# Optimization experiments

Hardware: AMD Instinct MI355X
Metric: run time of the kernel (lower is better)

Reference implementation:

```python
import jax, jax.numpy as jnp
from jax import lax
import numpy as np

BOHR = 0.52917721067  # Angstrom per Bohr (au.BOHR)
DAMP_MUTUAL = 0.39
DAMP_FIELD = 0.7
N_ITER = 7  # fixed-point iterations for induced dipoles


def setup_inputs() -> dict:
    key = jax.random.key(0)
    N = 100000
    deg = 32
    E = N * deg
    k1, k2, k3, k4, k5, k6, k7 = jax.random.split(key, 7)
    edge_src = jax.random.randint(k1, (E,), 0, N)
    edge_dst = jax.random.randint(k2, (E,), 0, N)
    # realistic interatomic distances in [1, 6] Angstrom (avoid r ~ 0)
    distances = 1.0 + 5.0 * jax.random.uniform(k3, (E,), dtype=jnp.float32)
    u = jax.random.normal(k4, (E, 3), dtype=jnp.float32)
    u = u / jnp.linalg.norm(u, axis=-1, keepdims=True)
    vec = u * distances[:, None]  # consistent |vec| == distances
    polarisability = 0.5 + 1.5 * jax.random.uniform(k5, (N,), dtype=jnp.float32)
    charges = 0.3 * jax.random.normal(k6, (N,), dtype=jnp.float32)
    species = jax.random.randint(k7, (N,), 1, 10)
    return {
        "species": species,
        "edge_src": edge_src,
        "edge_dst": edge_dst,
        "distances": distances,
        "vec": vec,
        "polarisability": polarisability,
        "charges": charges,
    }


def reference(species, edge_src, edge_dst, distances, vec, polarisability, charges):
    N = polarisability.shape[0]
    # convert to atomic units
    rij = distances / BOHR                      # [E]
    vec_ij = vec / BOHR                         # [E,3]
    pol = polarisability.reshape(-1) / BOHR**3  # [N]

    # Thole damping: u_ij^3 = r^3 / sqrt(alpha_i * alpha_j)
    alpha_ij = pol[edge_src] * pol[edge_dst]
    uij3 = rij**3 / jnp.sqrt(alpha_ij)
    exp_m = jnp.exp(-DAMP_MUTUAL * uij3)
    l3_m = 1.0 - exp_m
    l5_m = 1.0 - (1.0 + DAMP_MUTUAL * uij3) * exp_m
    l3_f = 1.0 - jnp.exp(-DAMP_FIELD * uij3)

    inv_r3 = 1.0 / rij**3
    inv_r5 = inv_r3 / rij**2

    # permanent (charge) electric field at src atoms, Thole-damped
    e_edges = (l3_f * charges[edge_dst] * inv_r3)[:, None] * vec_ij  # [E,3]
    E0 = jax.ops.segment_sum(e_edges, edge_src, num_segments=N)      # [N,3]

    alpha = pol[:, None]  # isotropic polarisability [N,1]

    def matvec(mu):
        # Thole-damped dipole-dipole interaction tensor applied to mu: (T mu)_i
        mu_d = mu[edge_dst]                                   # [E,3]
        dot = jnp.sum(vec_ij * mu_d, axis=-1)                 # [E]
        t = (l3_m * inv_r3)[:, None] * mu_d \
            - (3.0 * l5_m * inv_r5 * dot)[:, None] * vec_ij   # [E,3]
        return jax.ops.segment_sum(t, edge_src, num_segments=N)

    # iterative induced dipoles: mu = alpha * (E0 - T mu)
    mu0 = alpha * E0

    def step(mu, _):
        return alpha * (E0 - matvec(mu)), None

    mu, _ = lax.scan(step, mu0, None, length=N_ITER)

    # per-atom polarisation energy: -1/2 mu . E0
    energy = -0.5 * jnp.sum(mu * E0, axis=-1)  # [N]
    return energy
```

## Files before the change

### kernel.cpp

```cpp
#include <hip/hip_runtime.h>
#include <hip/hip_fp16.h>


static constexpr float INV_B  = 1.0f / 0.52917721067f;
static constexpr float INV_B3 = INV_B * INV_B * INV_B;
static constexpr float DM = 0.39f;
static constexpr float DF = 0.7f;
static constexpr int   NITER = 7;
#define SCAN_B 512
#define CHUNK 16384
#define BUILD_T 1024
#define MAXBUCK 512

__device__ inline unsigned packh2(float a, float b) {
    return (unsigned)__half_as_ushort(__float2half_rn(a)) |
           ((unsigned)__half_as_ushort(__float2half_rn(b)) << 16);
}
__device__ inline float unph_lo(unsigned u) {
    return __half2float(__ushort_as_half((unsigned short)(u & 0xFFFFu)));
}
__device__ inline float unph_hi(unsigned u) {
    return __half2float(__ushort_as_half((unsigned short)(u >> 16)));
}


__global__ void bhist_kernel(const int* __restrict__ esrc, int* __restrict__ hraw,
                             int* __restrict__ hpad, int E, int nbuck, int nblk)
{
    __shared__ int cnt[MAXBUCK];
    int tid = threadIdx.x, blk = blockIdx.x;
    for (int b = tid; b < nbuck; b += blockDim.x) cnt[b] = 0;
    __syncthreads();
    int lo = blk * CHUNK, hi = min(E, lo + CHUNK);
    for (int i = lo + tid; i < hi; i += blockDim.x)
        atomicAdd(&cnt[esrc[i] >> 8], 1);
    __syncthreads();
    for (int b = tid; b < nbuck; b += blockDim.x) {
        int c = cnt[b];
        hraw[b * nblk + blk] = c;
        hpad[b * nblk + blk] = (c + 7) & ~7;
    }
}


__global__ void scan1_kernel(const int* __restrict__ in, int* __restrict__ excl,
                             int* __restrict__ blocksum, int n)
{
    __shared__ int sh[SCAN_B];
    int tid = threadIdx.x;
    int i = blockIdx.x * SCAN_B + tid;
    int v = (i < n) ? in[i] : 0;
    sh[tid] = v;
    __syncthreads();
    for (int off = 1; off < SCAN_B; off <<= 1) {
        int t = (tid >= off) ? sh[tid - off] : 0;
        __syncthreads();
        sh[tid] += t;
        __syncthreads();
    }
    if (i < n) excl[i] = sh[tid] - v;
    if (tid == SCAN_B - 1) blocksum[blockIdx.x] = sh[tid];
}

__global__ void scan2_kernel(int* __restrict__ blocksum, int nb)
{
    __shared__ int sh[512];
    int tid = threadIdx.x;
    int v = (tid < nb) ? blocksum[tid] : 0;
    sh[tid] = v;
    __syncthreads();
    for (int off = 1; off < 512; off <<= 1) {
        int t = (tid >= off) ? sh[tid - off] : 0;
        __syncthreads();
        sh[tid] += t;
        __syncthreads();
    }
    if (tid < nb) blocksum[tid] = sh[tid] - v;
}

__global__ void scan3_kernel(int* __restrict__ excl, const int* __restrict__ blocksum, int n)
{
    int i = blockIdx.x * SCAN_B + threadIdx.x;
    if (i < n) excl[i] += blocksum[blockIdx.x];
}

__global__ void bktptr_kernel(const int* __restrict__ hoffpad, const int* __restrict__ hpad,
                              int* __restrict__ bktptr, int nbuck, int nblk, int nScan)
{
    int b = blockIdx.x * blockDim.x + threadIdx.x;
    if (b < nbuck) bktptr[b] = hoffpad[b * nblk];
    if (b == nbuck) bktptr[b] = hoffpad[nScan - 1] + hpad[nScan - 1];
}


__global__ void build_kernel(const int* __restrict__ esrc, const int* __restrict__ edst,
                             const float* __restrict__ dist, const float* __restrict__ vec,
                             const float* __restrict__ pol, const float* __restrict__ chg,
                             const int* __restrict__ hoffpad, const int* __restrict__ hpad,
                             uint4* __restrict__ recs, int E, int nbuck, int nblk)
{
    __shared__ int cur[MAXBUCK];
    int tid = threadIdx.x, blk = blockIdx.x;
    for (int b = tid; b < nbuck; b += blockDim.x) cur[b] = hoffpad[b * nblk + blk];
    __syncthreads();
    int lo = blk * CHUNK, hi = min(E, lo + CHUNK);
    for (int i = lo + tid; i < hi; i += blockDim.x) {
        int s = esrc[i], d = edst[i];
        float r  = dist[i] * INV_B;
        float vx = vec[3*i+0] * INV_B;
        float vy = vec[3*i+1] * INV_B;
        float vz = vec[3*i+2] * INV_B;
        float ps = pol[s] * INV_B3;
        float pd = pol[d] * INV_B3;
        float r2 = r * r;
        float r3 = r2 * r;
        float u  = r3 * rsqrtf(ps * pd);
        float em = __expf(-DM * u);
        float l3m = 1.0f - em;
        float l5m = 1.0f - (1.0f + DM * u) * em;
        float inv_r3 = 1.0f / r3;
        float inv_r5 = inv_r3 / r2;
        float c1 = l3m * inv_r3;
        float sw = sqrtf(3.0f * l5m * inv_r5);
        float ec = (1.0f - __expf(-DF * u)) * chg[d] * inv_r3;
        float g  = ec / sw;
        int slot = atomicAdd(&cur[s >> 8], 1);
        uint4 rc;
        rc.x = (unsigned)(d | ((s & 255) << 20));
        rc.y = __float_as_uint(c1);
        rc.z = packh2(sw * vx, sw * vy);
        rc.w = packh2(sw * vz, g);
        recs[slot] = rc;
    }
    __syncthreads();
    for (int b = tid; b < nbuck; b += blockDim.x) {
        int base = hoffpad[b * nblk + blk];
        int end  = base + hpad[b * nblk + blk];
        for (int s = cur[b]; s < end; ++s) recs[s] = make_uint4(0, 0, 0, 0);
    }
}


__global__ void sort_kernel(const int* __restrict__ bktptr, const int* __restrict__ hoffraw,
                            int nblk, const uint4* __restrict__ recs_raw,
                            unsigned* __restrict__ srt, float* __restrict__ gsrt,
                            int* __restrict__ rowbeg, int* __restrict__ rowend, int N)
{
    __shared__ int hist[256];
    __shared__ int scn[256];
    __shared__ int cur[256];
    int tid = threadIdx.x, b = blockIdx.x;
    int j0 = bktptr[b], j1 = bktptr[b + 1];
    int tight0 = hoffraw[b * nblk];
    if (tid < 256) hist[tid] = 0;
    __syncthreads();
    for (int j = j0 + tid; j < j1; j += blockDim.x) {
        uint4 rc = recs_raw[j];
        if (rc.y) atomicAdd(&hist[rc.x >> 20], 1);
    }
    __syncthreads();
    if (tid < 256) scn[tid] = hist[tid];
    __syncthreads();
    for (int off = 1; off < 256; off <<= 1) {
        int t = 0;
        if (tid < 256 && tid >= off) t = scn[tid - off];
        __syncthreads();
        if (tid < 256) scn[tid] += t;
        __syncthreads();
    }
    if (tid < 256) {
        int cnt = hist[tid];
        int beg = tight0 + scn[tid] - cnt;
        cur[tid] = beg;
        int row = b * 256 + tid;
        if (row < N) { rowbeg[row] = beg; rowend[row] = beg + cnt; }
    }
    __syncthreads();
    for (int j = j0 + tid; j < j1; j += blockDim.x) {
        uint4 rc = recs_raw[j];
        if (rc.y) {
            int slot = atomicAdd(&cur[rc.x >> 20], 1);
            float c1 = __uint_as_float(rc.y);
            float wx = unph_lo(rc.z);
            srt[3*slot+0] = rc.x;
            srt[3*slot+1] = packh2(c1, wx);
            srt[3*slot+2] = rc.w;
            srt[3*slot+2] = packh2(unph_hi(rc.z), unph_lo(rc.w));
            gsrt[slot] = unph_hi(rc.w);
        }
    }
}


__global__ void e0g_kernel(const int* __restrict__ rowbeg, const int* __restrict__ rowend,
                           const unsigned* __restrict__ srt, const float* __restrict__ gsrt,
                           const float* __restrict__ pol,
                           float4* __restrict__ E0, float4* __restrict__ mu, int N)
{
    int tid  = threadIdx.x;
    int lane = tid & 15;
    int row  = (blockIdx.x * blockDim.x + tid) >> 4;
    if (row >= N) return;
    int r0 = rowbeg[row], r1 = rowend[row];
    float sx = 0.f, sy = 0.f, sz = 0.f;
    for (int j = r0 + lane; j < r1; j += 16) {
        unsigned w0 = srt[3*j+1];
        unsigned w1 = srt[3*j+2];
        float g = gsrt[j];
        sx += g * unph_hi(w0);
        sy += g * unph_lo(w1);
        sz += g * unph_hi(w1);
    }
    for (int m = 8; m >= 1; m >>= 1) {
        sx += __shfl_xor(sx, m);
        sy += __shfl_xor(sy, m);
        sz += __shfl_xor(sz, m);
    }
    if (lane == 0) {
        E0[row] = make_float4(sx, sy, sz, 0.f);
        float a = pol[row] * INV_B3;
        mu[row] = make_float4(a * sx, a * sy, a * sz, 0.f);
    }
}

__global__ void mvg_kernel(const int* __restrict__ rowbeg, const int* __restrict__ rowend,
                           const unsigned* __restrict__ srt, const float4* __restrict__ E0,
                           const float* __restrict__ pol,
                           const float4* __restrict__ mu_in, float4* __restrict__ mu_out,
                           float* __restrict__ energy, int N, int final_iter)
{
    int tid  = threadIdx.x;
    int lane = tid & 15;
    int row  = (blockIdx.x * blockDim.x + tid) >> 4;
    if (row >= N) return;
    int r0 = rowbeg[row], r1 = rowend[row];
    float ax = 0.f, ay = 0.f, az = 0.f;
    for (int j = r0 + lane; j < r1; j += 16) {
        unsigned pk = srt[3*j+0];
        unsigned w0 = srt[3*j+1];
        unsigned w1 = srt[3*j+2];
        float4 m = mu_in[pk & 0xFFFFF];
        float c1 = unph_lo(w0);
        float wx = unph_hi(w0), wy = unph_lo(w1), wz = unph_hi(w1);
        float dot = wx * m.x + wy * m.y + wz * m.z;
        ax += c1 * m.x - dot * wx;
        ay += c1 * m.y - dot * wy;
        az += c1 * m.z - dot * wz;
    }
    for (int msk = 8; msk >= 1; msk >>= 1) {
        ax += __shfl_xor(ax, msk);
        ay += __shfl_xor(ay, msk);
        az += __shfl_xor(az, msk);
    }
    if (lane == 0) {
        float4 e0 = E0[row];
        float a = pol[row] * INV_B3;
        float mx = a * (e0.x - ax);
        float my = a * (e0.y - ay);
        float mz = a * (e0.z - az);
        mu_out[row] = make_float4(mx, my, mz, 0.f);
        if (final_iter)
            energy[row] = -0.5f * (mx * e0.x + my * e0.y + mz * e0.z);
    }
}


__global__ void e0b_kernel(const int* __restrict__ bktptr, const uint4* __restrict__ recs,
                           const float* __restrict__ pol,
                           float4* __restrict__ E0, float4* __restrict__ mu, int N)
{
    __shared__ float acc[256 * 3];
    int tid = threadIdx.x, b = blockIdx.x;
    for (int k = tid; k < 768; k += 256) acc[k] = 0.f;
    __syncthreads();
    int j0 = bktptr[b], j1 = bktptr[b + 1];
    for (int j = j0 + tid; j < j1; j += 256) {
        uint4 rc = recs[j];
        int lr = (int)(rc.x >> 20) & 255;
        float g = unph_hi(rc.w);
        atomicAdd(&acc[lr*3+0], g * unph_lo(rc.z));
        atomicAdd(&acc[lr*3+1], g * unph_hi(rc.z));
        atomicAdd(&acc[lr*3+2], g * unph_lo(rc.w));
    }
    __syncthreads();
    int r = b * 256 + tid;
    if (r < N) {
        float ax = acc[tid*3], ay = acc[tid*3+1], az = acc[tid*3+2];
        E0[r] = make_float4(ax, ay, az, 0.f);
        float a = pol[r] * INV_B3;
        mu[r] = make_float4(a * ax, a * ay, a * az, 0.f);
    }
}

__global__ void mvb_kernel(const int* __restrict__ bktptr, const uint4* __restrict__ recs,
                           const float4* __restrict__ E0, const float* __restrict__ pol,
                           const float4* __restrict__ mu_in, float4* __restrict__ mu_out,
                           float* __restrict__ energy, int N, int final_iter)
{
    __shared__ float acc[256 * 3];
    int tid = threadIdx.x, b = blockIdx.x;
    for (int k = tid; k < 768; k += 256) acc[k] = 0.f;
    __syncthreads();
    int j0 = bktptr[b], j1 = bktptr[b + 1];
    for (int j = j0 + tid; j < j1; j += 256) {
        uint4 rc = recs[j];
        float4 m = mu_in[rc.x & 0xFFFFF];
        float c1 = __uint_as_float(rc.y);
        float wx = unph_lo(rc.z), wy = unph_hi(rc.z), wz = unph_lo(rc.w);
        float dot = wx * m.x + wy * m.y + wz * m.z;
        int lr = (int)(rc.x >> 20) & 255;
        atomicAdd(&acc[lr*3+0], c1 * m.x - dot * wx);
        atomicAdd(&acc[lr*3+1], c1 * m.y - dot * wy);
        atomicAdd(&acc[lr*3+2], c1 * m.z - dot * wz);
    }
    __syncthreads();
    int r = b * 256 + tid;
    if (r < N) {
        float4 e0 = E0[r];
        float a = pol[r] * INV_B3;
        float mx = a * (e0.x - acc[tid*3+0]);
        float my = a * (e0.y - acc[tid*3+1]);
        float mz = a * (e0.z - acc[tid*3+2]);
        mu_out[r] = make_float4(mx, my, mz, 0.f);
        if (final_iter)
            energy[r] = -0.5f * (mx * e0.x + my * e0.y + mz * e0.z);
    }
}


__global__ void fb_e0_kernel(const int* esrc, const int* edst, const float* dist,
                             const float* vec, const float* pol, const float* chg,
                             float4* E0, int E)
{
    int e = blockIdx.x * blockDim.x + threadIdx.x;
    if (e >= E) return;
    int s = esrc[e], d = edst[e];
    float r  = dist[e] * INV_B;
    float vx = vec[3*e+0]*INV_B, vy = vec[3*e+1]*INV_B, vz = vec[3*e+2]*INV_B;
    float r3 = r*r*r;
    float u  = r3 * rsqrtf(pol[s]*INV_B3 * pol[d]*INV_B3);
    float ec = (1.0f - __expf(-DF*u)) * chg[d] / r3;
    atomicAdd(&E0[s].x, ec*vx); atomicAdd(&E0[s].y, ec*vy); atomicAdd(&E0[s].z, ec*vz);
}

__global__ void fb_init_kernel(const float* pol, const float4* E0, float4* mu, float4* acc, int N)
{
    int i = blockIdx.x * blockDim.x + threadIdx.x;
    if (i >= N) return;
    float a = pol[i]*INV_B3; float4 e0 = E0[i];
    mu[i]  = make_float4(a*e0.x, a*e0.y, a*e0.z, 0.f);
    acc[i] = make_float4(0.f,0.f,0.f,0.f);
}

__global__ void fb_matvec_kernel(const int* esrc, const int* edst, const float* dist,
                                 const float* vec, const float* pol,
                                 const float4* mu, float4* acc, int E)
{
    int e = blockIdx.x * blockDim.x + threadIdx.x;
    if (e >= E) return;
    int s = esrc[e], d = edst[e];
    float r  = dist[e]*INV_B;
    float vx = vec[3*e+0]*INV_B, vy = vec[3*e+1]*INV_B, vz = vec[3*e+2]*INV_B;
    float r2 = r*r, r3 = r2*r;
    float u  = r3 * rsqrtf(pol[s]*INV_B3 * pol[d]*INV_B3);
    float em = __expf(-DM*u);
    float c1 = (1.0f - em) / r3;
    float c2 = 3.0f * (1.0f - (1.0f + DM*u)*em) / (r3*r2);
    float4 m = mu[d];
    float k = c2 * (vx*m.x + vy*m.y + vz*m.z);
    atomicAdd(&acc[s].x, c1*m.x - k*vx);
    atomicAdd(&acc[s].y, c1*m.y - k*vy);
    atomicAdd(&acc[s].z, c1*m.z - k*vz);
}

__global__ void fb_update_kernel(const float* pol, const float4* E0, float4* acc,
                                 float4* mu, float* energy, int N, int final_iter)
{
    int i = blockIdx.x * blockDim.x + threadIdx.x;
    if (i >= N) return;
    float a = pol[i]*INV_B3; float4 e0 = E0[i]; float4 ac = acc[i];
    float mx = a*(e0.x-ac.x), my = a*(e0.y-ac.y), mz = a*(e0.z-ac.z);
    mu[i]  = make_float4(mx,my,mz,0.f);
    acc[i] = make_float4(0.f,0.f,0.f,0.f);
    if (final_iter) energy[i] = -0.5f*(mx*e0.x + my*e0.y + mz*e0.z);
}


static inline size_t align_up(size_t x, size_t a) { return (x + a - 1) & ~(a - 1); }

extern "C" void kernel_launch(void* const* d_in, const int* in_sizes, int n_in,
                              void* d_out, int out_size, void* d_ws, size_t ws_size,
                              hipStream_t stream)
{
    const int*   esrc = (const int*)  d_in[1];
    const int*   edst = (const int*)  d_in[2];
    const float* dist = (const float*)d_in[3];
    const float* vec  = (const float*)d_in[4];
    const float* pol  = (const float*)d_in[5];
    const float* chg  = (const float*)d_in[6];
    const int E = in_sizes[1];
    const int N = in_sizes[5];
    float* out = (float*)d_out;

    const int nbuck = (N + 255) >> 8;
    const int nblk  = (E + CHUNK - 1) / CHUNK;
    const int nScan = nbuck * nblk;
    const int g1    = (nScan + SCAN_B - 1) / SCAN_B;
    const size_t Epad = (size_t)E + 7u * (size_t)nScan;

    char* ws = (char*)d_ws;
    size_t off = 0;
    auto carve = [&](size_t bytes) { size_t o = off; off = align_up(off + bytes, 256); return o; };
    size_t o_hpad    = carve((size_t)nScan * 4);
    size_t o_hoffpad = carve((size_t)nScan * 4);
    size_t o_bsum1   = carve(512 * 4);
    size_t o_bkt     = carve((size_t)(nbuck + 1) * 4);
    size_t o_E0      = carve((size_t)N * 16);
    size_t o_mua     = carve((size_t)N * 16);
    size_t o_mub     = carve((size_t)N * 16);
    size_t o_hraw    = carve((size_t)nScan * 4);
    size_t o_recsraw = carve(Epad * 16);
    size_t need_mid  = off;
    size_t o_hoffraw = carve((size_t)nScan * 4);
    size_t o_bsum2   = carve(512 * 4);
    size_t o_rowbeg  = carve((size_t)N * 4);
    size_t o_rowend  = carve((size_t)N * 4);
    size_t o_srt     = carve((size_t)E * 12);
    size_t o_gsrt    = carve((size_t)E * 4);
    size_t need_sort = off;

    bool shape_ok = (nbuck <= MAXBUCK) && (g1 <= 512) && (nbuck >= 1) && (N < (1 << 20));
    bool ok_sort = shape_ok && (ws_size >= need_sort);
    bool ok_mid  = shape_ok && (ws_size >= need_mid);

    if (ok_sort || ok_mid) {
        int*    hpad    = (int*)   (ws + o_hpad);
        int*    hoffpad = (int*)   (ws + o_hoffpad);
        int*    bsum1   = (int*)   (ws + o_bsum1);
        int*    bktptr  = (int*)   (ws + o_bkt);
        float4* E0      = (float4*)(ws + o_E0);
        float4* mu_a    = (float4*)(ws + o_mua);
        float4* mu_b    = (float4*)(ws + o_mub);
        int*    hraw    = (int*)   (ws + o_hraw);
        uint4*  recsraw = (uint4*) (ws + o_recsraw);

        bhist_kernel<<<nblk, BUILD_T, 0, stream>>>(esrc, hraw, hpad, E, nbuck, nblk);
        scan1_kernel<<<g1, SCAN_B, 0, stream>>>(hpad, hoffpad, bsum1, nScan);
        scan2_kernel<<<1, 512, 0, stream>>>(bsum1, g1);
        scan3_kernel<<<g1, SCAN_B, 0, stream>>>(hoffpad, bsum1, nScan);
        bktptr_kernel<<<(nbuck + 256) / 256, 256, 0, stream>>>(hoffpad, hpad, bktptr,
                                                               nbuck, nblk, nScan);
        build_kernel<<<nblk, BUILD_T, 0, stream>>>(esrc, edst, dist, vec, pol, chg,
                                                   hoffpad, hpad, recsraw, E, nbuck, nblk);

        if (ok_sort) {
            int*      hoffraw = (int*)     (ws + o_hoffraw);
            int*      bsum2   = (int*)     (ws + o_bsum2);
            int*      rowbeg  = (int*)     (ws + o_rowbeg);
            int*      rowend  = (int*)     (ws + o_rowend);
            unsigned* srt     = (unsigned*)(ws + o_srt);
            float*    gsrt    = (float*)   (ws + o_gsrt);

            scan1_kernel<<<g1, SCAN_B, 0, stream>>>(hraw, hoffraw, bsum2, nScan);
            scan2_kernel<<<1, 512, 0, stream>>>(bsum2, g1);
            scan3_kernel<<<g1, SCAN_B, 0, stream>>>(hoffraw, bsum2, nScan);
            sort_kernel<<<nbuck, 512, 0, stream>>>(bktptr, hoffraw, nblk, recsraw,
                                                   srt, gsrt, rowbeg, rowend, N);

            const int NG16 = (N + 15) / 16;
            e0g_kernel<<<NG16, 256, 0, stream>>>(rowbeg, rowend, srt, gsrt, pol, E0, mu_a, N);
            float4* min_ = mu_a; float4* mout_ = mu_b;
            for (int it = 0; it < NITER; ++it) {
                mvg_kernel<<<NG16, 256, 0, stream>>>(rowbeg, rowend, srt, E0, pol,
                                                     min_, mout_, out, N, it == NITER - 1);
                float4* t = min_; min_ = mout_; mout_ = t;
            }
        } else {
            e0b_kernel<<<nbuck, 256, 0, stream>>>(bktptr, recsraw, pol, E0, mu_a, N);
            float4* min_ = mu_a; float4* mout_ = mu_b;
            for (int it = 0; it < NITER; ++it) {
                mvb_kernel<<<nbuck, 256, 0, stream>>>(bktptr, recsraw, E0, pol,
                                                      min_, mout_, out, N, it == NITER - 1);
                float4* t = min_; min_ = mout_; mout_ = t;
            }
        }
    } else {
        float4* E0  = (float4*)(ws);
        float4* mu  = (float4*)(ws + (size_t)N * 16);
        float4* acc = (float4*)(ws + (size_t)N * 32);
        const int EB = 256, NB = 256;
        const int EG = (E + EB - 1) / EB;
        const int NG = (N + NB - 1) / NB;
        hipMemsetAsync(E0, 0, (size_t)N * 16, stream);
        fb_e0_kernel<<<EG, EB, 0, stream>>>(esrc, edst, dist, vec, pol, chg, E0, E);
        fb_init_kernel<<<NG, NB, 0, stream>>>(pol, E0, mu, acc, N);
        for (int it = 0; it < NITER; ++it) {
            fb_matvec_kernel<<<EG, EB, 0, stream>>>(esrc, edst, dist, vec, pol, mu, acc, E);
            fb_update_kernel<<<NG, NB, 0, stream>>>(pol, E0, acc, mu, out, N, it == NITER - 1);
        }
    }
}
```

Measured before the change: 336.6 us.

## Locally sort edges by bucket in shared memory before building records

The build kernel now builds a per-block histogram and prefix scan of source buckets, creates a shared-memory permutation, and processes edges in bucket order so each thread writes its record to a deterministic, contiguous slot. This replaces the scattered global stores ordered by atomics with mostly coalesced writes into each bucket's region, and the padding fill now uses a rounded-up count instead of the hpad array. The cost is an extra pass over esrc, roughly 40KB of shared memory per block that limits occupancy, and permuted (less coalesced) input reads. A redundant store in the sort kernel is also removed.

```diff
diff --git a/kernel.cpp b/kernel.cpp
--- a/kernel.cpp
+++ b/kernel.cpp
@@ -93,23 +93,58 @@
 }
 
 
-__global__ void build_kernel(const int* __restrict__ esrc, const int* __restrict__ edst,
-                             const float* __restrict__ dist, const float* __restrict__ vec,
-                             const float* __restrict__ pol, const float* __restrict__ chg,
-                             const int* __restrict__ hoffpad, const int* __restrict__ hpad,
-                             uint4* __restrict__ recs, int E, int nbuck, int nblk)
-{
-    __shared__ int cur[MAXBUCK];
+__global__ __launch_bounds__(BUILD_T)
+void build_kernel(const int* __restrict__ esrc, const int* __restrict__ edst,
+                  const float* __restrict__ dist, const float* __restrict__ vec,
+                  const float* __restrict__ pol, const float* __restrict__ chg,
+                  const int* __restrict__ hoffpad,
+                  uint4* __restrict__ recs, int E, int nbuck, int nblk)
+{
+    __shared__ unsigned short perm[CHUNK];
+    __shared__ int hist[MAXBUCK];
+    __shared__ int scn[MAXBUCK];
+    __shared__ int lscan[MAXBUCK];
+    __shared__ int lcur[MAXBUCK];
+    __shared__ int rbase[MAXBUCK];
     int tid = threadIdx.x, blk = blockIdx.x;
-    for (int b = tid; b < nbuck; b += blockDim.x) cur[b] = hoffpad[b * nblk + blk];
-    __syncthreads();
-    int lo = blk * CHUNK, hi = min(E, lo + CHUNK);
-    for (int i = lo + tid; i < hi; i += blockDim.x) {
-        int s = esrc[i], d = edst[i];
-        float r  = dist[i] * INV_B;
-        float vx = vec[3*i+0] * INV_B;
-        float vy = vec[3*i+1] * INV_B;
-        float vz = vec[3*i+2] * INV_B;
+    int lo = blk * CHUNK, hi = min(E, lo + CHUNK), cnt = hi - lo;
+
+    for (int b = tid; b < nbuck; b += BUILD_T) hist[b] = 0;
+    __syncthreads();
+    for (int i = tid; i < cnt; i += BUILD_T)
+        atomicAdd(&hist[esrc[lo + i] >> 8], 1);
+    __syncthreads();
+    if (tid < MAXBUCK) scn[tid] = (tid < nbuck) ? hist[tid] : 0;
+    __syncthreads();
+    for (int off = 1; off < MAXBUCK; off <<= 1) {
+        int t = 0;
+        if (tid < MAXBUCK && tid >= off) t = scn[tid - off];
+        __syncthreads();
+        if (tid < MAXBUCK) scn[tid] += t;
+        __syncthreads();
+    }
+    if (tid < nbuck) {
+        int excl = scn[tid] - hist[tid];
+        lscan[tid] = excl;
+        lcur[tid]  = excl;
+        rbase[tid] = hoffpad[tid * nblk + blk];
+    }
+    __syncthreads();
+    for (int i = tid; i < cnt; i += BUILD_T) {
+        int b = esrc[lo + i] >> 8;
+        int sl = atomicAdd(&lcur[b], 1);
+        perm[sl] = (unsigned short)i;
+    }
+    __syncthreads();
+    for (int k = tid; k < cnt; k += BUILD_T) {
+        int i  = perm[k];
+        int gi = lo + i;
+        int s = esrc[gi], d = edst[gi];
+        int b = s >> 8;
+        float r  = dist[gi] * INV_B;
+        float vx = vec[3*gi+0] * INV_B;
+        float vy = vec[3*gi+1] * INV_B;
+        float vz = vec[3*gi+2] * INV_B;
         float ps = pol[s] * INV_B3;
         float pd = pol[d] * INV_B3;
         float r2 = r * r;
@@ -124,19 +159,19 @@
         float sw = sqrtf(3.0f * l5m * inv_r5);
         float ec = (1.0f - __expf(-DF * u)) * chg[d] * inv_r3;
         float g  = ec / sw;
-        int slot = atomicAdd(&cur[s >> 8], 1);
         uint4 rc;
         rc.x = (unsigned)(d | ((s & 255) << 20));
         rc.y = __float_as_uint(c1);
         rc.z = packh2(sw * vx, sw * vy);
         rc.w = packh2(sw * vz, g);
-        recs[slot] = rc;
-    }
-    __syncthreads();
-    for (int b = tid; b < nbuck; b += blockDim.x) {
-        int base = hoffpad[b * nblk + blk];
-        int end  = base + hpad[b * nblk + blk];
-        for (int s = cur[b]; s < end; ++s) recs[s] = make_uint4(0, 0, 0, 0);
+        recs[rbase[b] + (k - lscan[b])] = rc;
+    }
+    __syncthreads();
+    for (int b = tid; b < nbuck; b += BUILD_T) {
+        int base = rbase[b];
+        int c    = hist[b];
+        int end  = base + ((c + 7) & ~7);
+        for (int s2 = base + c; s2 < end; ++s2) recs[s2] = make_uint4(0, 0, 0, 0);
     }
 }
 
@@ -169,11 +204,11 @@
         __syncthreads();
     }
     if (tid < 256) {
-        int cnt = hist[tid];
-        int beg = tight0 + scn[tid] - cnt;
+        int c = hist[tid];
+        int beg = tight0 + scn[tid] - c;
         cur[tid] = beg;
         int row = b * 256 + tid;
-        if (row < N) { rowbeg[row] = beg; rowend[row] = beg + cnt; }
+        if (row < N) { rowbeg[row] = beg; rowend[row] = beg + c; }
     }
     __syncthreads();
     for (int j = j0 + tid; j < j1; j += blockDim.x) {
@@ -181,10 +216,8 @@
         if (rc.y) {
             int slot = atomicAdd(&cur[rc.x >> 20], 1);
             float c1 = __uint_as_float(rc.y);
-            float wx = unph_lo(rc.z);
             srt[3*slot+0] = rc.x;
-            srt[3*slot+1] = packh2(c1, wx);
-            srt[3*slot+2] = rc.w;
+            srt[3*slot+1] = packh2(c1, unph_lo(rc.z));
             srt[3*slot+2] = packh2(unph_hi(rc.z), unph_lo(rc.w));
             gsrt[slot] = unph_hi(rc.w);
         }
@@ -451,7 +484,7 @@
         bktptr_kernel<<<(nbuck + 256) / 256, 256, 0, stream>>>(hoffpad, hpad, bktptr,
                                                                nbuck, nblk, nScan);
         build_kernel<<<nblk, BUILD_T, 0, stream>>>(esrc, edst, dist, vec, pol, chg,
-                                                   hoffpad, hpad, recsraw, E, nbuck, nblk);
+                                                   hoffpad, recsraw, E, nbuck, nblk);
 
         if (ok_sort) {
             int*      hoffraw = (int*)     (ws + o_hoffraw);
```

Measured after the change: 435.9 us. +29.5%, slower.
